# Kernel optimization log

Hardware: AMD Instinct MI355X
Metric: run time of the kernel (lower is better)

## Reference

```python
import jax, jax.numpy as jnp
import numpy as np

B, S, D, H = 2, 2048, 1024, 16
HD = D // H  # head_dim = 64


def setup_inputs() -> dict:
    key = jax.random.key(0)
    ks = jax.random.split(key, 11)
    init = 1.0 / np.sqrt(D)
    inp = {
        "query": jax.random.normal(ks[0], (B, S, D), jnp.float32),
        "key": jax.random.normal(ks[1], (B, S, D), jnp.float32),
        "value": jax.random.normal(ks[2], (B, S, D), jnp.float32),
        "Wq": jax.random.uniform(ks[3], (D, D), jnp.float32, -init, init),
        "bq": jax.random.uniform(ks[4], (D,), jnp.float32, -init, init),
        "Wk": jax.random.uniform(ks[5], (D, D), jnp.float32, -init, init),
        "bk": jax.random.uniform(ks[6], (D,), jnp.float32, -init, init),
        "Wv": jax.random.uniform(ks[7], (D, D), jnp.float32, -init, init),
        "bv": jax.random.uniform(ks[8], (D,), jnp.float32, -init, init),
        "Wo": jax.random.uniform(ks[9], (D, D), jnp.float32, -init, init),
        "bo": jax.random.uniform(ks[10], (D,), jnp.float32, -init, init),
    }
    return inp


def reference(query, key, value, Wq, bq, Wk, bk, Wv, bv, Wo, bo):
    # Linear projections (torch Linear: x @ W.T + b)
    q = query @ Wq.T + bq  # [B,S,D]
    k = key @ Wk.T + bk
    v = value @ Wv.T + bv
    # split heads -> [B,H,S,HD]
    q = q.reshape(B, S, H, HD).transpose(0, 2, 1, 3)
    k = k.reshape(B, S, H, HD).transpose(0, 2, 1, 3)
    v = v.reshape(B, S, H, HD).transpose(0, 2, 1, 3)
    # NOTE: original code divides by scale = head_dim**-0.5, i.e. multiplies
    # scores by sqrt(head_dim). Reproduced faithfully.
    scale = HD ** (-0.5)
    scores = jnp.einsum("bhqd,bhkd->bhqk", q, k) / scale  # [B,H,S,S]
    attn = jax.nn.softmax(scores, axis=-1)
    x = jnp.einsum("bhqk,bhkd->bhqd", attn, v)  # [B,H,S,HD]
    x = x.transpose(0, 2, 1, 3).reshape(B, S, D)
    return x @ Wo.T + bo
```

## Files before the change

### kernel.cpp

```cpp
#include <hip/hip_runtime.h>
#include <stdint.h>
#include <stddef.h>

#define SCALE_LOG2E 11.541560327111707f
#define E8 4194304
#define M1 1048576
#define NROW 65536

typedef __attribute__((ext_vector_type(8))) _Float16 f16x8;
typedef __attribute__((ext_vector_type(4))) _Float16 f16x4;
typedef __attribute__((ext_vector_type(4))) float f32x4;

#if __has_builtin(__builtin_amdgcn_exp2f)
#define EXP2F(x) __builtin_amdgcn_exp2f(x)
#else
#define EXP2F(x) exp2f(x)
#endif

__device__ __forceinline__ f32x4 mfma_f16(f16x8 a, f16x8 b, f32x4 c) {
  return __builtin_amdgcn_mfma_f32_16x16x32_f16(a, b, c, 0, 0, 0);
}

__device__ __forceinline__ f32x4 mfma16_f16(f16x4 a, f16x4 b, f32x4 c) {
  return __builtin_amdgcn_mfma_f32_16x16x16f16(a, b, c, 0, 0, 0);
}

__device__ __forceinline__ void async16(const void* g, void* lds) {
  __builtin_amdgcn_global_load_lds(
      (const __attribute__((address_space(1))) unsigned int*)g,
      (__attribute__((address_space(3))) unsigned int*)lds, 16, 0, 0);
}

__global__ void prep_all(const float* __restrict__ q, const float* __restrict__ k,
                         const float* __restrict__ v,
                         const float* __restrict__ wq, const float* __restrict__ wk,
                         const float* __restrict__ wv, const float* __restrict__ wo,
                         _Float16* __restrict__ Xf, _Float16* __restrict__ Wf) {
  const int gid = blockIdx.x;
  const float* src;
  _Float16* dst;
  int i;
  if (gid < 12288) {
    const int z = gid >> 12;
    src = (z == 0) ? q : (z == 1) ? k : v;
    dst = Xf + (size_t)z * E8;
    i = (gid & 4095) * 256 + threadIdx.x;
  } else {
    const int g2 = gid - 12288;
    const int z = g2 >> 10;
    src = (z == 0) ? wq : (z == 1) ? wk : (z == 2) ? wv : wo;
    dst = Wf + (size_t)z * M1;
    i = (g2 & 1023) * 256 + threadIdx.x;
  }
  float4 x = ((const float4*)src)[i];
  f16x4 h = {(_Float16)x.x, (_Float16)x.y, (_Float16)x.z, (_Float16)x.w};
  ((f16x4*)dst)[i] = h;
}

__global__ __launch_bounds__(256, 3) void gemm_qkv(
    const _Float16* __restrict__ Xf,
    const _Float16* __restrict__ Wf,
    const float* __restrict__ bq, const float* __restrict__ bk,
    const float* __restrict__ bv,
    _Float16* __restrict__ Of)
{
  __shared__ _Float16 SMEM[16384];
  _Float16* LA = SMEM;
  _Float16* LB = SMEM + 8192;
  const int z = blockIdx.z;
  const int tid = threadIdx.x;
  const int lane = tid & 63;
  const int wv = tid >> 6;
  const int wm = wv >> 1, wn = wv & 1;
  const int rl = lane & 15, qd = lane >> 4;
  const int m0 = blockIdx.y * 128, n0 = blockIdx.x * 128;

  const _Float16* A0 = Xf + (size_t)z * E8;
  const _Float16* W0 = Wf + (size_t)z * M1;
  const float* bias = (z == 0) ? bq : (z == 1) ? bk : bv;

  f32x4 acc[4][4];
#pragma unroll
  for (int i = 0; i < 4; i++)
#pragma unroll
    for (int j = 0; j < 4; j++) acc[i][j] = f32x4{0.f, 0.f, 0.f, 0.f};

  const int srow = wv * 32 + (lane >> 2);
  const int scol = (lane & 3) * 8;

  auto stage = [&](int k0, int buf) {
    const _Float16* ga = A0 + (size_t)(m0 + srow) * 1024 + k0 + scol;
    async16(ga, &LA[buf * 4096 + wv * 1024]);
    async16(ga + 16 * 1024, &LA[buf * 4096 + wv * 1024 + 512]);
    const _Float16* gb = W0 + (size_t)(n0 + srow) * 1024 + k0 + scol;
    async16(gb, &LB[buf * 4096 + wv * 1024]);
    async16(gb + 16 * 1024, &LB[buf * 4096 + wv * 1024 + 512]);
  };

  stage(0, 0);
  for (int t = 0; t < 32; t++) {
    const int buf = t & 1;
    __syncthreads();
    if (t + 1 < 32) stage((t + 1) * 32, buf ^ 1);
    f16x8 af[4], bfr[4];
#pragma unroll
    for (int i = 0; i < 4; i++) af[i] = *(const f16x8*)&LA[buf * 4096 + (wm * 64 + i * 16 + rl) * 32 + qd * 8];
#pragma unroll
    for (int j = 0; j < 4; j++) bfr[j] = *(const f16x8*)&LB[buf * 4096 + (wn * 64 + j * 16 + rl) * 32 + qd * 8];
#pragma unroll
    for (int i = 0; i < 4; i++)
#pragma unroll
      for (int j = 0; j < 4; j++) acc[i][j] = mfma_f16(af[i], bfr[j], acc[i][j]);
  }

  if (z == 2) {
#pragma unroll
    for (int j = 0; j < 4; j++) {
      const int nn = n0 + wn * 64 + j * 16 + rl;
      const float bj = bias[nn];
      const int hh = nn >> 6, e = nn & 63;
#pragma unroll
      for (int i = 0; i < 4; i++) {
        const int mm = m0 + wm * 64 + i * 16 + qd * 4;
        const int b = mm >> 11, s = mm & 2047;
        f16x4 pk = {(_Float16)(acc[i][j][0] + bj), (_Float16)(acc[i][j][1] + bj),
                    (_Float16)(acc[i][j][2] + bj), (_Float16)(acc[i][j][3] + bj)};
        *(f16x4*)(Of + 2 * (size_t)E8 + (((size_t)((b * 16 + hh) * 64 + e)) << 11) + s) = pk;
      }
    }
  } else {
    const float scl = (z == 0) ? SCALE_LOG2E : 1.0f;
    _Float16* base = Of + (size_t)z * E8;
    __syncthreads();
#pragma unroll
    for (int j = 0; j < 4; j++) {
      const int nl = wn * 64 + j * 16 + rl;
      const float bj = bias[n0 + nl];
#pragma unroll
      for (int i = 0; i < 4; i++) {
        const int ml = wm * 64 + i * 16 + qd * 4;
        const int np = nl ^ (qd << 4);
#pragma unroll
        for (int r = 0; r < 4; r++)
          SMEM[(ml + r) * 128 + np] = (_Float16)((acc[i][j][r] + bj) * scl);
      }
    }
    __syncthreads();
#pragma unroll
    for (int it2 = 0; it2 < 8; it2++) {
      const int m = (it2 * 256 + tid) >> 4;
      const int col8 = (tid & 15) * 8;
      const int np = col8 ^ (((m >> 2) & 3) << 4);
      f16x8 vrow = *(const f16x8*)&SMEM[m * 128 + np];
      const int sg = m0 + m;
      const int b = sg >> 11, s = sg & 2047;
      const int nn = n0 + col8;
      const int hh = nn >> 6, e = nn & 63;
      *(f16x8*)(base + (((size_t)((b * 16 + hh) * 2048 + s)) << 6) + e) = vrow;
    }
  }
}

__global__ __launch_bounds__(256, 4) void attn_kernel(
    const _Float16* __restrict__ Qb,
    const _Float16* __restrict__ Kb,
    const _Float16* __restrict__ Vt,
    float* __restrict__ Op,
    float2* __restrict__ ML)
{
  __shared__ _Float16 Ks[2][4096];
  __shared__ _Float16 Vs[2][4096];
  const int tid = threadIdx.x;
  const int lane = tid & 63;
  const int wv = tid >> 6;
  const int rl = lane & 15, qd = lane >> 4;
  const int bh = blockIdx.z;
  const int half = blockIdx.y;
  const int kvb = half * 1024;
  const int q0 = blockIdx.x * 128 + wv * 32;

  f16x8 qf[2][2];
#pragma unroll
  for (int mt = 0; mt < 2; mt++)
#pragma unroll
    for (int kk = 0; kk < 2; kk++)
      qf[mt][kk] = *(const f16x8*)(Qb + ((size_t)bh * 2048 + q0 + mt * 16 + rl) * 64 +
                                   kk * 32 + qd * 8);

  float m_[2] = {-1e30f, -1e30f};
  f32x4 lacc[2];
  f32x4 o[2][4];
#pragma unroll
  for (int mt = 0; mt < 2; mt++) {
    lacc[mt] = f32x4{0.f, 0.f, 0.f, 0.f};
#pragma unroll
    for (int jt = 0; jt < 4; jt++) o[mt][jt] = f32x4{0.f, 0.f, 0.f, 0.f};
  }
  const f16x4 ones = {(_Float16)1.f, (_Float16)1.f, (_Float16)1.f, (_Float16)1.f};

  auto stage = [&](int kv, int buf) {
#pragma unroll
    for (int it = 0; it < 2; it++) {
      const int cI = it * 256 + tid;
      const int row = cI >> 3;
      const int c = (cI & 7) ^ (row & 7);
      const int dst = (it * 256 + wv * 64) * 8;
      async16(Kb + ((size_t)bh * 2048 + kv + row) * 64 + c * 8, &Ks[buf][dst]);
      async16(Vt + ((size_t)bh * 64 + row) * 2048 + kv + c * 8, &Vs[buf][dst]);
    }
  };

  stage(kvb, 0);

  for (int t = 0; t < 16; t++) {
    const int buf = t & 1;
    __syncthreads();
    if (t + 1 < 16) stage(kvb + (t + 1) * 64, buf ^ 1);

    f32x4 sc[2][4];
#pragma unroll
    for (int mt = 0; mt < 2; mt++)
#pragma unroll
      for (int nt = 0; nt < 4; nt++) sc[mt][nt] = f32x4{0.f, 0.f, 0.f, 0.f};
    __builtin_amdgcn_s_setprio(1);
#pragma unroll
    for (int nt = 0; nt < 4; nt++) {
      const int ro = (nt * 16 + rl) * 64;
#pragma unroll
      for (int kk = 0; kk < 2; kk++) {
        const int cc = (((kk * 4 + qd) ^ (rl & 7)) << 3);
        f16x8 kh = *(const f16x8*)&Ks[buf][ro + cc];
#pragma unroll
        for (int mt = 0; mt < 2; mt++)
          sc[mt][nt] = mfma_f16(kh, qf[mt][kk], sc[mt][nt]);
      }
    }
    __builtin_amdgcn_s_setprio(0);

    f16x4 pf[2][4];
#pragma unroll
    for (int mt = 0; mt < 2; mt++) {
      float g0 = fmaxf(fmaxf(sc[mt][0][0], sc[mt][0][1]), sc[mt][0][2]);
      float g1 = fmaxf(fmaxf(sc[mt][0][3], sc[mt][1][0]), sc[mt][1][1]);
      float g2 = fmaxf(fmaxf(sc[mt][1][2], sc[mt][1][3]), sc[mt][2][0]);
      float g3 = fmaxf(fmaxf(sc[mt][2][1], sc[mt][2][2]), sc[mt][2][3]);
      float g4 = fmaxf(fmaxf(sc[mt][3][0], sc[mt][3][1]), sc[mt][3][2]);
      float h0 = fmaxf(fmaxf(g0, g1), g2);
      float mloc = fmaxf(fmaxf(h0, g3), fmaxf(g4, sc[mt][3][3]));
      float mx = fmaxf(mloc, __shfl_xor(mloc, 16));
      mx = fmaxf(mx, __shfl_xor(mx, 32));
#pragma unroll
      for (int nt = 0; nt < 4; nt++)
#pragma unroll
        for (int r = 0; r < 4; r++) sc[mt][nt][r] = EXP2F(sc[mt][nt][r] - mloc);
      const float mold = m_[mt];
      float mnew = mold;
      if (__any(mx > mold + 8.f)) {
        mnew = fmaxf(mold, mx);
        const float al = EXP2F(mold - mnew);
#pragma unroll
        for (int r = 0; r < 4; r++) lacc[mt][r] *= al;
#pragma unroll
        for (int jt = 0; jt < 4; jt++)
#pragma unroll
          for (int r = 0; r < 4; r++) o[mt][jt][r] *= al;
        m_[mt] = mnew;
      }
      const float cf = EXP2F(mloc - mnew);
#pragma unroll
      for (int nt = 0; nt < 4; nt++)
        pf[mt][nt] = f16x4{(_Float16)(sc[mt][nt][0] * cf), (_Float16)(sc[mt][nt][1] * cf),
                           (_Float16)(sc[mt][nt][2] * cf), (_Float16)(sc[mt][nt][3] * cf)};
    }

    __builtin_amdgcn_s_setprio(1);
#pragma unroll
    for (int mt = 0; mt < 2; mt++)
#pragma unroll
      for (int nt = 0; nt < 4; nt++)
        lacc[mt] = mfma16_f16(ones, pf[mt][nt], lacc[mt]);
#pragma unroll
    for (int nt = 0; nt < 4; nt++) {
      const int cb = nt * 2 + (qd >> 1);
#pragma unroll
      for (int jt = 0; jt < 4; jt++) {
        const int row = jt * 16 + rl;
        f16x4 vvv = *(const f16x4*)&Vs[buf][row * 64 + ((cb ^ (rl & 7)) << 3) + (qd & 1) * 4];
        o[0][jt] = mfma16_f16(vvv, pf[0][nt], o[0][jt]);
        o[1][jt] = mfma16_f16(vvv, pf[1][nt], o[1][jt]);
      }
    }
    __builtin_amdgcn_s_setprio(0);
  }

#pragma unroll
  for (int mt = 0; mt < 2; mt++) {
    const size_t row = (size_t)bh * 2048 + q0 + mt * 16 + rl;
    float* op = Op + ((size_t)half * NROW + row) * 64;
#pragma unroll
    for (int jt = 0; jt < 4; jt++)
      *(f32x4*)(op + jt * 16 + qd * 4) = o[mt][jt];
    if (qd == 0) ML[(size_t)half * NROW + row] = make_float2(m_[mt], lacc[mt][0]);
  }
}

__global__ void merge_kernel(const float* __restrict__ Op,
                             const float2* __restrict__ ML,
                             _Float16* __restrict__ Xo) {
  const int t = threadIdx.x;
  const int row = blockIdx.x * 16 + (t >> 4);
  const int d0 = (t & 15) * 4;
  const float2 ml1 = ML[row];
  const float2 ml2 = ML[NROW + row];
  const float m = fmaxf(ml1.x, ml2.x);
  const float w1 = EXP2F(ml1.x - m), w2 = EXP2F(ml2.x - m);
  const float inv = 1.0f / (ml1.y * w1 + ml2.y * w2);
  const float4 o1 = *(const float4*)(Op + (size_t)row * 64 + d0);
  const float4 o2 = *(const float4*)(Op + (size_t)NROW * 64 + (size_t)row * 64 + d0);
  const int bh = row >> 11, q = row & 2047;
  const int b = bh >> 4, hh = bh & 15;
  f16x4 pk = {(_Float16)((o1.x * w1 + o2.x * w2) * inv),
              (_Float16)((o1.y * w1 + o2.y * w2) * inv),
              (_Float16)((o1.z * w1 + o2.z * w2) * inv),
              (_Float16)((o1.w * w1 + o2.w * w2) * inv)};
  *(f16x4*)(Xo + ((size_t)(b * 2048 + q)) * 1024 + hh * 64 + d0) = pk;
}

__global__ __launch_bounds__(256, 2) void gemm_out(
    const _Float16* __restrict__ A0,
    const _Float16* __restrict__ W0,
    const float* __restrict__ bias,
    float* __restrict__ out)
{
  __shared__ _Float16 LA[2][2048];
  __shared__ _Float16 LB[2][4096];
  const int tid = threadIdx.x;
  const int lane = tid & 63;
  const int wv = tid >> 6;
  const int wm = wv >> 1, wn = wv & 1;
  const int rl = lane & 15, qd = lane >> 4;
  const int m0 = blockIdx.y * 64, n0 = blockIdx.x * 128;

  f32x4 acc[2][4];
#pragma unroll
  for (int i = 0; i < 2; i++)
#pragma unroll
    for (int j = 0; j < 4; j++) acc[i][j] = f32x4{0.f, 0.f, 0.f, 0.f};

  auto stage = [&](int k0, int buf) {
    {
      const int row = tid >> 2, c = tid & 3;
      async16(A0 + (size_t)(m0 + row) * 1024 + k0 + c * 8, &LA[buf][wv * 512]);
    }
#pragma unroll
    for (int it = 0; it < 2; it++) {
      const int cI = it * 256 + tid;
      const int row = cI >> 2, c = cI & 3;
      async16(W0 + (size_t)(n0 + row) * 1024 + k0 + c * 8,
              &LB[buf][it * 2048 + wv * 512]);
    }
  };

  stage(0, 0);
  for (int t = 0; t < 32; t++) {
    const int buf = t & 1;
    __syncthreads();
    if (t + 1 < 32) stage((t + 1) * 32, buf ^ 1);
    f16x8 af[2], bfr[4];
#pragma unroll
    for (int i = 0; i < 2; i++) af[i] = *(const f16x8*)&LA[buf][(wm * 32 + i * 16 + rl) * 32 + qd * 8];
#pragma unroll
    for (int j = 0; j < 4; j++) bfr[j] = *(const f16x8*)&LB[buf][(wn * 64 + j * 16 + rl) * 32 + qd * 8];
#pragma unroll
    for (int i = 0; i < 2; i++)
#pragma unroll
      for (int j = 0; j < 4; j++) acc[i][j] = mfma_f16(af[i], bfr[j], acc[i][j]);
  }

#pragma unroll
  for (int j = 0; j < 4; j++) {
    const int nn = n0 + wn * 64 + j * 16 + rl;
    const float bj = bias[nn];
#pragma unroll
    for (int i = 0; i < 2; i++) {
      const int mm = m0 + wm * 32 + i * 16 + qd * 4;
#pragma unroll
      for (int r = 0; r < 4; r++)
        out[(size_t)(mm + r) * 1024 + nn] = acc[i][j][r] + bj;
    }
  }
}

extern "C" void kernel_launch(void* const* d_in, const int* in_sizes, int n_in,
                              void* d_out, int out_size, void* d_ws, size_t ws_size,
                              hipStream_t stream) {
  const float* query = (const float*)d_in[0];
  const float* key   = (const float*)d_in[1];
  const float* value = (const float*)d_in[2];
  const float* Wq = (const float*)d_in[3];
  const float* bq = (const float*)d_in[4];
  const float* Wk = (const float*)d_in[5];
  const float* bk = (const float*)d_in[6];
  const float* Wv = (const float*)d_in[7];
  const float* bv = (const float*)d_in[8];
  const float* Wo = (const float*)d_in[9];
  const float* bo = (const float*)d_in[10];

  _Float16* ws = (_Float16*)d_ws;
  _Float16* Xf = ws;
  _Float16* Wf = ws + 3 * (size_t)E8;
  _Float16* Qh = Wf + 4 * (size_t)M1;
  _Float16* Kh = Qh + (size_t)E8;
  _Float16* Vt = Kh + (size_t)E8;
  _Float16* Xa = Vt + (size_t)E8;
  float*    Op = (float*)(Xa + (size_t)E8);
  float2*   ML = (float2*)(Op + 2 * (size_t)NROW * 64);

  prep_all<<<16384, 256, 0, stream>>>(query, key, value, Wq, Wk, Wv, Wo, Xf, Wf);
  gemm_qkv<<<dim3(8, 32, 3), 256, 0, stream>>>(Xf, Wf, bq, bk, bv, Qh);
  attn_kernel<<<dim3(16, 2, 32), 256, 0, stream>>>(Qh, Kh, Vt, Op, ML);
  merge_kernel<<<4096, 256, 0, stream>>>(Op, ML, Xa);
  gemm_out<<<dim3(8, 64), 256, 0, stream>>>(Xa, Wf + 3 * (size_t)M1, bo, (float*)d_out);
}
```

Measured before the change: 251.5 us.

## Drop split-KV attention and merge kernel; normalize in attention epilogue

The attention kernel no longer splits the KV sequence into two halves. Each block now walks all 2048 keys and normalizes its own output, writing fp16 straight into the head-merged layout. This removes the merge kernel, the fp32 partial-output and max/sum buffers, and one launch. The row sum is now built with VALU adds plus shuffles instead of MFMA against a ones vector. The cost is half as many attention blocks (512 instead of 1024), each with a serial loop twice as long, which reduces parallelism across CUs.

```diff
diff --git a/kernel.cpp b/kernel.cpp
--- a/kernel.cpp
+++ b/kernel.cpp
@@ -5,7 +5,6 @@
 #define SCALE_LOG2E 11.541560327111707f
 #define E8 4194304
 #define M1 1048576
-#define NROW 65536
 
 typedef __attribute__((ext_vector_type(8))) _Float16 f16x8;
 typedef __attribute__((ext_vector_type(4))) _Float16 f16x4;
@@ -165,8 +164,7 @@
     const _Float16* __restrict__ Qb,
     const _Float16* __restrict__ Kb,
     const _Float16* __restrict__ Vt,
-    float* __restrict__ Op,
-    float2* __restrict__ ML)
+    _Float16* __restrict__ Xo)
 {
   __shared__ _Float16 Ks[2][4096];
   __shared__ _Float16 Vs[2][4096];
@@ -174,9 +172,7 @@
   const int lane = tid & 63;
   const int wv = tid >> 6;
   const int rl = lane & 15, qd = lane >> 4;
-  const int bh = blockIdx.z;
-  const int half = blockIdx.y;
-  const int kvb = half * 1024;
+  const int bh = blockIdx.y;
   const int q0 = blockIdx.x * 128 + wv * 32;
 
   f16x8 qf[2][2];
@@ -187,16 +183,12 @@
       qf[mt][kk] = *(const f16x8*)(Qb + ((size_t)bh * 2048 + q0 + mt * 16 + rl) * 64 +
                                    kk * 32 + qd * 8);
 
-  float m_[2] = {-1e30f, -1e30f};
-  f32x4 lacc[2];
+  float m_[2] = {-1e30f, -1e30f}, l_[2] = {0.f, 0.f};
   f32x4 o[2][4];
 #pragma unroll
-  for (int mt = 0; mt < 2; mt++) {
-    lacc[mt] = f32x4{0.f, 0.f, 0.f, 0.f};
+  for (int mt = 0; mt < 2; mt++)
 #pragma unroll
     for (int jt = 0; jt < 4; jt++) o[mt][jt] = f32x4{0.f, 0.f, 0.f, 0.f};
-  }
-  const f16x4 ones = {(_Float16)1.f, (_Float16)1.f, (_Float16)1.f, (_Float16)1.f};
 
   auto stage = [&](int kv, int buf) {
 #pragma unroll
@@ -210,12 +202,12 @@
     }
   };
 
-  stage(kvb, 0);
-
-  for (int t = 0; t < 16; t++) {
+  stage(0, 0);
+
+  for (int t = 0; t < 32; t++) {
     const int buf = t & 1;
     __syncthreads();
-    if (t + 1 < 16) stage(kvb + (t + 1) * 64, buf ^ 1);
+    if (t + 1 < 32) stage((t + 1) * 64, buf ^ 1);
 
     f32x4 sc[2][4];
 #pragma unroll
@@ -245,21 +237,24 @@
       float g2 = fmaxf(fmaxf(sc[mt][1][2], sc[mt][1][3]), sc[mt][2][0]);
       float g3 = fmaxf(fmaxf(sc[mt][2][1], sc[mt][2][2]), sc[mt][2][3]);
       float g4 = fmaxf(fmaxf(sc[mt][3][0], sc[mt][3][1]), sc[mt][3][2]);
-      float h0 = fmaxf(fmaxf(g0, g1), g2);
-      float mloc = fmaxf(fmaxf(h0, g3), fmaxf(g4, sc[mt][3][3]));
+      float mloc = fmaxf(fmaxf(fmaxf(g0, g1), g2), fmaxf(fmaxf(g3, g4), sc[mt][3][3]));
       float mx = fmaxf(mloc, __shfl_xor(mloc, 16));
       mx = fmaxf(mx, __shfl_xor(mx, 32));
+      float sm = 0.f;
 #pragma unroll
       for (int nt = 0; nt < 4; nt++)
 #pragma unroll
-        for (int r = 0; r < 4; r++) sc[mt][nt][r] = EXP2F(sc[mt][nt][r] - mloc);
+        for (int r = 0; r < 4; r++) {
+          float p = EXP2F(sc[mt][nt][r] - mloc);
+          sc[mt][nt][r] = p;
+          sm += p;
+        }
       const float mold = m_[mt];
       float mnew = mold;
       if (__any(mx > mold + 8.f)) {
         mnew = fmaxf(mold, mx);
         const float al = EXP2F(mold - mnew);
-#pragma unroll
-        for (int r = 0; r < 4; r++) lacc[mt][r] *= al;
+        l_[mt] *= al;
 #pragma unroll
         for (int jt = 0; jt < 4; jt++)
 #pragma unroll
@@ -267,6 +262,7 @@
         m_[mt] = mnew;
       }
       const float cf = EXP2F(mloc - mnew);
+      l_[mt] += sm * cf;
 #pragma unroll
       for (int nt = 0; nt < 4; nt++)
         pf[mt][nt] = f16x4{(_Float16)(sc[mt][nt][0] * cf), (_Float16)(sc[mt][nt][1] * cf),
@@ -274,11 +270,6 @@
     }
 
     __builtin_amdgcn_s_setprio(1);
-#pragma unroll
-    for (int mt = 0; mt < 2; mt++)
-#pragma unroll
-      for (int nt = 0; nt < 4; nt++)
-        lacc[mt] = mfma16_f16(ones, pf[mt][nt], lacc[mt]);
 #pragma unroll
     for (int nt = 0; nt < 4; nt++) {
       const int cb = nt * 2 + (qd >> 1);
@@ -293,37 +284,21 @@
     __builtin_amdgcn_s_setprio(0);
   }
 
+  const int b = bh >> 4, hh = bh & 15;
 #pragma unroll
   for (int mt = 0; mt < 2; mt++) {
-    const size_t row = (size_t)bh * 2048 + q0 + mt * 16 + rl;
-    float* op = Op + ((size_t)half * NROW + row) * 64;
-#pragma unroll
-    for (int jt = 0; jt < 4; jt++)
-      *(f32x4*)(op + jt * 16 + qd * 4) = o[mt][jt];
-    if (qd == 0) ML[(size_t)half * NROW + row] = make_float2(m_[mt], lacc[mt][0]);
-  }
-}
-
-__global__ void merge_kernel(const float* __restrict__ Op,
-                             const float2* __restrict__ ML,
-                             _Float16* __restrict__ Xo) {
-  const int t = threadIdx.x;
-  const int row = blockIdx.x * 16 + (t >> 4);
-  const int d0 = (t & 15) * 4;
-  const float2 ml1 = ML[row];
-  const float2 ml2 = ML[NROW + row];
-  const float m = fmaxf(ml1.x, ml2.x);
-  const float w1 = EXP2F(ml1.x - m), w2 = EXP2F(ml2.x - m);
-  const float inv = 1.0f / (ml1.y * w1 + ml2.y * w2);
-  const float4 o1 = *(const float4*)(Op + (size_t)row * 64 + d0);
-  const float4 o2 = *(const float4*)(Op + (size_t)NROW * 64 + (size_t)row * 64 + d0);
-  const int bh = row >> 11, q = row & 2047;
-  const int b = bh >> 4, hh = bh & 15;
-  f16x4 pk = {(_Float16)((o1.x * w1 + o2.x * w2) * inv),
-              (_Float16)((o1.y * w1 + o2.y * w2) * inv),
-              (_Float16)((o1.z * w1 + o2.z * w2) * inv),
-              (_Float16)((o1.w * w1 + o2.w * w2) * inv)};
-  *(f16x4*)(Xo + ((size_t)(b * 2048 + q)) * 1024 + hh * 64 + d0) = pk;
+    float lt = l_[mt] + __shfl_xor(l_[mt], 16);
+    lt += __shfl_xor(lt, 32);
+    const float inv = 1.0f / lt;
+    const int s = q0 + mt * 16 + rl;
+    _Float16* xp = Xo + ((size_t)(b * 2048 + s)) * 1024 + hh * 64;
+#pragma unroll
+    for (int jt = 0; jt < 4; jt++) {
+      f16x4 pk = {(_Float16)(o[mt][jt][0] * inv), (_Float16)(o[mt][jt][1] * inv),
+                  (_Float16)(o[mt][jt][2] * inv), (_Float16)(o[mt][jt][3] * inv)};
+      *(f16x4*)(xp + jt * 16 + qd * 4) = pk;
+    }
+  }
 }
 
 __global__ __launch_bounds__(256, 2) void gemm_out(
@@ -413,12 +388,9 @@
   _Float16* Kh = Qh + (size_t)E8;
   _Float16* Vt = Kh + (size_t)E8;
   _Float16* Xa = Vt + (size_t)E8;
-  float*    Op = (float*)(Xa + (size_t)E8);
-  float2*   ML = (float2*)(Op + 2 * (size_t)NROW * 64);
 
   prep_all<<<16384, 256, 0, stream>>>(query, key, value, Wq, Wk, Wv, Wo, Xf, Wf);
   gemm_qkv<<<dim3(8, 32, 3), 256, 0, stream>>>(Xf, Wf, bq, bk, bv, Qh);
-  attn_kernel<<<dim3(16, 2, 32), 256, 0, stream>>>(Qh, Kh, Vt, Op, ML);
-  merge_kernel<<<4096, 256, 0, stream>>>(Op, ML, Xa);
+  attn_kernel<<<dim3(16, 32), 256, 0, stream>>>(Qh, Kh, Vt, Xa);
   gemm_out<<<dim3(8, 64), 256, 0, stream>>>(Xa, Wf + 3 * (size_t)M1, bo, (float*)d_out);
 }
```

New measurement: 248.5 us. Within noise of the previous version (-1.2%).
